# Kernel optimization log

Hardware: AMD Instinct MI355X
Metric: run time of the kernel (lower is better)

## Reference

```python
import jax, jax.numpy as jnp
import numpy as np

DELTA = 16
L_S = 32
HID = 8      # fast SSM hidden dim
GH = 64      # slow GRU hidden
OD = 2 * HID # slow branch output dim


def setup_inputs() -> dict:
    key = jax.random.key(0)
    ks = jax.random.split(key, 9)
    B, T = 128, 65536
    x = jax.random.normal(ks[0], (B, T), dtype=jnp.float32)
    # fast branch params: f_in: Linear(1, HID, bias=False); f_out: Linear(HID, 1, bias=False)
    w_in = jax.random.normal(ks[1], (HID,), dtype=jnp.float32) * 0.3
    w_out = jax.random.normal(ks[2], (HID,), dtype=jnp.float32) * 0.3
    # slow branch GRU (input_size=1) + output linear
    w_ih = jax.random.normal(ks[3], (3 * GH,), dtype=jnp.float32) * 0.1
    w_hh = jax.random.normal(ks[4], (3 * GH, GH), dtype=jnp.float32) * 0.1
    b_ih = jax.random.normal(ks[5], (3 * GH,), dtype=jnp.float32) * 0.1
    b_hh = jax.random.normal(ks[6], (3 * GH,), dtype=jnp.float32) * 0.1
    w_sl = jax.random.normal(ks[7], (OD, GH), dtype=jnp.float32) * 0.1
    b_sl = jax.random.normal(ks[8], (OD,), dtype=jnp.float32) * 0.1
    return {"x": x, "w_in": w_in, "w_out": w_out, "w_ih": w_ih, "w_hh": w_hh,
            "b_ih": b_ih, "b_hh": b_hh, "w_sl": w_sl, "b_sl": b_sl}


def _slow_branch(frames, w_ih, w_hh, b_ih, b_hh, w_sl, b_sl):
    # frames: (B, F, L_S). GRU over the L_S samples of each frame, last hidden -> Linear.
    B, F, L = frames.shape
    seq = frames.reshape(B * F, L).T  # (L, B*F), time-major

    def gru_step(h, xt):
        gi = xt[:, None] * w_ih[None, :] + b_ih          # (N, 3GH)
        gh = h @ w_hh.T + b_hh                            # (N, 3GH)
        ir, iz, inn = jnp.split(gi, 3, axis=-1)
        hr, hz, hn = jnp.split(gh, 3, axis=-1)
        r = jax.nn.sigmoid(ir + hr)
        z = jax.nn.sigmoid(iz + hz)
        n = jnp.tanh(inn + r * hn)
        h = (1.0 - z) * n + z * h
        return h, None

    h0 = jnp.zeros((B * F, GH), dtype=frames.dtype)
    hT, _ = jax.lax.scan(gru_step, h0, seq)
    eps = hT @ w_sl.T + b_sl                              # (B*F, OD)
    return eps.reshape(B, F, OD)


def reference(x, w_in, w_out, w_ih, w_hh, b_ih, b_hh, w_sl, b_sl):
    B, T = x.shape
    F = (T - L_S) // DELTA + 1
    # x.unfold(1, 32, delta) -> gather frames (B, F, L_S)
    idx = jnp.arange(F)[:, None] * DELTA + jnp.arange(L_S)[None, :]
    frames = x[:, idx]                                    # (B, F, L_S)
    eps = _slow_branch(frames, w_ih, w_hh, b_ih, b_hh, w_sl, b_sl)
    A_s = jax.nn.sigmoid(eps[..., :HID])                  # (B, F, H)
    g_s = eps[..., HID:]                                  # (B, F, H)
    # per-timestep frame index j = clamp(i // delta - 1, 0)
    j = jnp.clip(jnp.arange(T) // DELTA - 1, 0, F - 1)
    A_t = A_s[:, j]                                       # (B, T, H)
    g_t = g_s[:, j]                                       # (B, T, H)
    # x_emb = f_in(x) * g  (f_in has no bias)
    u_t = x[:, :, None] * w_in[None, None, :] * g_t       # (B, T, H)

    def step(h, inp):
        A, u = inp
        h = A * h + u
        return h, h

    h0 = jnp.zeros((B, HID), dtype=x.dtype)
    _, hs = jax.lax.scan(step, h0, (A_t.transpose(1, 0, 2), u_t.transpose(1, 0, 2)))  # hs: (T, B, H)
    y = jnp.einsum('tbh,h->bt', hs, w_out)                # f_out, no bias
    return y
```

## Files before the change

kernel.cpp:

```cpp
#include <hip/hip_runtime.h>
#include <hip/hip_bf16.h>
#include <math.h>

#define B_SZ 128
#define T_SZ 65536
#define F_FR 4095
#define GHID 64
#define HID 8
#define CHUNK 256
#define NCH (T_SZ / CHUNK)

typedef _Float16 half8 __attribute__((ext_vector_type(8)));
typedef float f32x4 __attribute__((ext_vector_type(4)));

#define L2E 1.4426950408889634f

static __device__ __forceinline__ float frcp(float v) {
#if __has_builtin(__builtin_amdgcn_rcpf)
    return __builtin_amdgcn_rcpf(v);
#else
    return 1.0f / v;
#endif
}
static __device__ __forceinline__ float fexp2(float v) {
#if __has_builtin(__builtin_amdgcn_exp2f)
    return __builtin_amdgcn_exp2f(v);
#else
    return exp2f(v);
#endif
}
__device__ __forceinline__ float sigm(float xv) { return frcp(1.0f + fexp2(-L2E * xv)); }

#define FSTR 68
#define XSTR 34

__global__ __launch_bounds__(256)
void gru_mfma(
    const float* __restrict__ x, const float* __restrict__ w_ih,
    const float* __restrict__ w_hh, const float* __restrict__ b_ih,
    const float* __restrict__ b_hh, const float* __restrict__ w_sl,
    const float* __restrict__ b_sl, float* __restrict__ ag)
{
    __shared__ _Float16 wlds[24 * 64 * 8];
    __shared__ float hx[4][32 * FSTR + 32 * XSTR];
    const int tid  = threadIdx.x;
    const int wv   = tid >> 6;
    const int lane = tid & 63;
    const int c16  = lane & 15;
    const int g    = lane >> 4;
    float* hb = &hx[wv][0];
    float* xs = hb + 32 * FSTR;
    const int tile = ((int)blockIdx.x * 4 + wv) * 32;

#pragma unroll
    for (int f = 0; f < 24; f += 4) {
        const int fi = f + wv;
        const int n = fi >> 1, c = fi & 1;
        const float sc = (n < 8) ? -L2E : (2.0f * L2E);
        const float* wp = w_hh + (16 * n + c16) * 64 + 32 * c + 8 * g;
        const float4 q0 = *(const float4*)wp;
        const float4 q1 = *(const float4*)(wp + 4);
        half8 w8;
        w8[0] = (_Float16)(sc * q0.x); w8[1] = (_Float16)(sc * q0.y);
        w8[2] = (_Float16)(sc * q0.z); w8[3] = (_Float16)(sc * q0.w);
        w8[4] = (_Float16)(sc * q1.x); w8[5] = (_Float16)(sc * q1.y);
        w8[6] = (_Float16)(sc * q1.z); w8[7] = (_Float16)(sc * q1.w);
        *(half8*)(wlds + (fi * 64 + lane) * 8) = w8;
    }

    float wiR[4], wiZ[4], wiN[4], bR[4], bZ[4], biN[4], bhN[4];
#pragma unroll
    for (int m = 0; m < 4; ++m) {
        const int j = c16 + 16 * m;
        wiR[m] = -L2E * w_ih[j];
        wiZ[m] = -L2E * w_ih[64 + j];
        wiN[m] = 2.0f * L2E * w_ih[128 + j];
        bR[m]  = -L2E * (b_ih[j] + b_hh[j]);
        bZ[m]  = -L2E * (b_ih[64 + j] + b_hh[64 + j]);
        biN[m] = 2.0f * L2E * b_ih[128 + j];
        bhN[m] = 2.0f * L2E * b_hh[128 + j];
    }

    {
        const int sl = lane & 31, half = lane >> 5;
        const int s = tile + sl;
        const int b = s / F_FR;
        const int f = s % F_FR;
        const float* xp = x + (long)b * T_SZ + f * 16 + 16 * half;
        const float4 p0 = *(const float4*)xp;
        const float4 p1 = *(const float4*)(xp + 4);
        const float4 p2 = *(const float4*)(xp + 8);
        const float4 p3 = *(const float4*)(xp + 12);
        float* xd = xs + sl * XSTR + 16 * half;
        *(float4*)(xd)      = p0;  *(float4*)(xd + 4)  = p1;
        *(float4*)(xd + 8)  = p2;  *(float4*)(xd + 12) = p3;
    }
    for (int idx = lane; idx < 32 * FSTR; idx += 64) hb[idx] = 0.0f;
    __syncthreads();

    float ho[2][4][4];
#pragma unroll
    for (int mt = 0; mt < 2; ++mt)
#pragma unroll
        for (int m = 0; m < 4; ++m)
#pragma unroll
            for (int r = 0; r < 4; ++r) ho[mt][m][r] = 0.0f;

#pragma unroll 1
    for (int t = 0; t < 32; ++t) {
        half8 ah[2][2], al[2][2];
#pragma unroll
        for (int mt = 0; mt < 2; ++mt)
#pragma unroll
        for (int c = 0; c < 2; ++c) {
            const float* rp = hb + (c16 + 16 * mt) * FSTR + 32 * c + 8 * g;
            const float4 u0 = *(const float4*)rp;
            const float4 u1 = *(const float4*)(rp + 4);
            const float fv[8] = {u0.x, u0.y, u0.z, u0.w, u1.x, u1.y, u1.z, u1.w};
#pragma unroll
            for (int e = 0; e < 8; ++e) {
                const _Float16 hi = (_Float16)fv[e];
                ah[mt][c][e] = hi;
                al[mt][c][e] = (_Float16)(fv[e] - (float)hi);
            }
        }
        float xt4[2][4];
#pragma unroll
        for (int mt = 0; mt < 2; ++mt)
#pragma unroll
        for (int r = 0; r < 4; ++r) xt4[mt][r] = xs[(4 * g + r + 16 * mt) * XSTR + t];

#pragma unroll
        for (int m = 0; m < 4; ++m) {
            f32x4 aR[2], aZ[2], aN[2];
#pragma unroll
            for (int mt = 0; mt < 2; ++mt) {
                aR[mt] = f32x4{bR[m], bR[m], bR[m], bR[m]};
                aZ[mt] = f32x4{bZ[m], bZ[m], bZ[m], bZ[m]};
                aN[mt] = f32x4{bhN[m], bhN[m], bhN[m], bhN[m]};
            }
#pragma unroll
            for (int c = 0; c < 2; ++c) {
                const half8 bfR = *(const half8*)(wlds + ((2 * m + c)       * 64 + lane) * 8);
                const half8 bfZ = *(const half8*)(wlds + ((2 * (4 + m) + c) * 64 + lane) * 8);
                const half8 bfN = *(const half8*)(wlds + ((2 * (8 + m) + c) * 64 + lane) * 8);
#pragma unroll
                for (int mt = 0; mt < 2; ++mt) {
                    aR[mt] = __builtin_amdgcn_mfma_f32_16x16x32_f16(ah[mt][c], bfR, aR[mt], 0, 0, 0);
                    aR[mt] = __builtin_amdgcn_mfma_f32_16x16x32_f16(al[mt][c], bfR, aR[mt], 0, 0, 0);
                    aZ[mt] = __builtin_amdgcn_mfma_f32_16x16x32_f16(ah[mt][c], bfZ, aZ[mt], 0, 0, 0);
                    aZ[mt] = __builtin_amdgcn_mfma_f32_16x16x32_f16(al[mt][c], bfZ, aZ[mt], 0, 0, 0);
                    aN[mt] = __builtin_amdgcn_mfma_f32_16x16x32_f16(ah[mt][c], bfN, aN[mt], 0, 0, 0);
                    aN[mt] = __builtin_amdgcn_mfma_f32_16x16x32_f16(al[mt][c], bfN, aN[mt], 0, 0, 0);
                }
            }
            const int jm = c16 + 16 * m;
#pragma unroll
            for (int mt = 0; mt < 2; ++mt) {
#pragma unroll
                for (int r = 0; r < 4; ++r) {
                    const float uR = fmaf(xt4[mt][r], wiR[m], aR[mt][r]);
                    const float rr = frcp(1.0f + fexp2(uR));
                    const float uZ = fmaf(xt4[mt][r], wiZ[m], aZ[mt][r]);
                    const float zf = frcp(1.0f + fexp2(uZ));
                    const float uN = fmaf(rr, aN[mt][r], fmaf(xt4[mt][r], wiN[m], biN[m]));
                    const float nn = fmaf(-2.0f, frcp(1.0f + fexp2(uN)), 1.0f);
                    const float hnew = fmaf(zf, ho[mt][m][r] - nn, nn);
                    ho[mt][m][r] = hnew;
                    hb[(4 * g + r + 16 * mt) * FSTR + jm] = hnew;
                }
            }
        }
    }

    const f32x4 zz = {0.0f, 0.0f, 0.0f, 0.0f};
    half8 wsl[2];
#pragma unroll
    for (int c = 0; c < 2; ++c) {
        const float4 q0 = *(const float4*)(w_sl + c16 * 64 + 32 * c + 8 * g);
        const float4 q1 = *(const float4*)(w_sl + c16 * 64 + 32 * c + 8 * g + 4);
        wsl[c][0] = (_Float16)q0.x; wsl[c][1] = (_Float16)q0.y;
        wsl[c][2] = (_Float16)q0.z; wsl[c][3] = (_Float16)q0.w;
        wsl[c][4] = (_Float16)q1.x; wsl[c][5] = (_Float16)q1.y;
        wsl[c][6] = (_Float16)q1.z; wsl[c][7] = (_Float16)q1.w;
    }
    const float bs = b_sl[c16];
#pragma unroll
    for (int mt = 0; mt < 2; ++mt) {
        half8 fh[2], fl[2];
#pragma unroll
        for (int c = 0; c < 2; ++c) {
            const float* rp = hb + (c16 + 16 * mt) * FSTR + 32 * c + 8 * g;
            const float4 u0 = *(const float4*)rp;
            const float4 u1 = *(const float4*)(rp + 4);
            const float fv[8] = {u0.x, u0.y, u0.z, u0.w, u1.x, u1.y, u1.z, u1.w};
#pragma unroll
            for (int e = 0; e < 8; ++e) {
                const _Float16 hi = (_Float16)fv[e];
                fh[c][e] = hi;
                fl[c][e] = (_Float16)(fv[e] - (float)hi);
            }
        }
        f32x4 ec = __builtin_amdgcn_mfma_f32_16x16x32_f16(fh[0], wsl[0], zz, 0, 0, 0);
        ec = __builtin_amdgcn_mfma_f32_16x16x32_f16(fl[0], wsl[0], ec, 0, 0, 0);
        ec = __builtin_amdgcn_mfma_f32_16x16x32_f16(fh[1], wsl[1], ec, 0, 0, 0);
        ec = __builtin_amdgcn_mfma_f32_16x16x32_f16(fl[1], wsl[1], ec, 0, 0, 0);
#pragma unroll
        for (int r = 0; r < 4; ++r) {
            float e = ec[r] + bs;
            if (c16 < 8) e = sigm(e);
            ag[(long)(tile + 16 * mt + 4 * g + r) * 16 + c16] = e;
        }
    }
}

__global__ __launch_bounds__(256) void fast_chunk(
    const float* __restrict__ x, const float* __restrict__ ag,
    const float* __restrict__ w_in,
    float* __restrict__ chP, float* __restrict__ chH)
{
    const int tid = blockIdx.x * 256 + threadIdx.x;
    const int b = tid / NCH, c = tid % NCH;
    float h[HID], P[HID];
#pragma unroll
    for (int i = 0; i < HID; ++i) { h[i] = 0.0f; P[i] = 1.0f; }
    const float* xp = x + (long)b * T_SZ + c * CHUNK;

#pragma unroll 1
    for (int g = 0; g < CHUNK / 16; ++g) {
        const int t0 = c * CHUNK + g * 16;
        int fr = t0 / 16 - 1; fr = max(0, min(F_FR - 1, fr));
        const float4* agp = (const float4*)(ag + ((long)b * F_FR + fr) * 16);
        const float4 a0 = agp[0], a1 = agp[1], g0 = agp[2], g1 = agp[3];
        const float A[HID]  = {a0.x, a0.y, a0.z, a0.w, a1.x, a1.y, a1.z, a1.w};
        const float Gv[HID] = {g0.x, g0.y, g0.z, g0.w, g1.x, g1.y, g1.z, g1.w};
        float wg[HID];
#pragma unroll
        for (int i = 0; i < HID; ++i) wg[i] = w_in[i] * Gv[i];
#pragma unroll
        for (int tt = 0; tt < 16; ++tt) {
            const float xt = xp[g * 16 + tt];
#pragma unroll
            for (int i = 0; i < HID; ++i) h[i] = fmaf(A[i], h[i], xt * wg[i]);
        }
#pragma unroll
        for (int i = 0; i < HID; ++i) {
            const float a2 = A[i] * A[i]; const float a4 = a2 * a2; const float a8 = a4 * a4;
            P[i] *= a8 * a8;
        }
    }
    float* pp = chP + (long)tid * HID;
    float* hp = chH + (long)tid * HID;
#pragma unroll
    for (int i = 0; i < HID; ++i) { pp[i] = P[i]; hp[i] = h[i]; }
}

__global__ __launch_bounds__(256) void chunk_scan(
    const float* __restrict__ chP, const float* __restrict__ chH,
    float* __restrict__ st)
{
    const int tid = blockIdx.x * 256 + threadIdx.x;
    if (tid >= B_SZ * HID) return;
    const int b = tid / HID, i = tid % HID;
    float h = 0.0f;
#pragma unroll 1
    for (int c = 0; c < NCH; ++c) {
        const long idx = ((long)b * NCH + c) * HID + i;
        st[idx] = h;
        h = fmaf(chP[idx], h, chH[idx]);
    }
}

__global__ __launch_bounds__(256) void fast_apply(
    const float* __restrict__ x, const float* __restrict__ ag,
    const float* __restrict__ w_in, const float* __restrict__ w_out,
    const float* __restrict__ st, float* __restrict__ y)
{
    const int tid = blockIdx.x * 256 + threadIdx.x;
    const int b = tid / NCH, c = tid % NCH;
    float h[HID];
    const float* sp = st + (long)tid * HID;
#pragma unroll
    for (int i = 0; i < HID; ++i) h[i] = sp[i];
    float wo[HID];
#pragma unroll
    for (int i = 0; i < HID; ++i) wo[i] = w_out[i];
    const float* xp = x + (long)b * T_SZ + c * CHUNK;
    float* yp = y + (long)b * T_SZ + c * CHUNK;

#pragma unroll 1
    for (int g = 0; g < CHUNK / 16; ++g) {
        const int t0 = c * CHUNK + g * 16;
        int fr = t0 / 16 - 1; fr = max(0, min(F_FR - 1, fr));
        const float4* agp = (const float4*)(ag + ((long)b * F_FR + fr) * 16);
        const float4 a0 = agp[0], a1 = agp[1], g0 = agp[2], g1 = agp[3];
        const float A[HID]  = {a0.x, a0.y, a0.z, a0.w, a1.x, a1.y, a1.z, a1.w};
        const float Gv[HID] = {g0.x, g0.y, g0.z, g0.w, g1.x, g1.y, g1.z, g1.w};
        float wg[HID];
#pragma unroll
        for (int i = 0; i < HID; ++i) wg[i] = w_in[i] * Gv[i];
#pragma unroll
        for (int tt = 0; tt < 16; ++tt) {
            const float xt = xp[g * 16 + tt];
            float acc = 0.0f;
#pragma unroll
            for (int i = 0; i < HID; ++i) {
                h[i] = fmaf(A[i], h[i], xt * wg[i]);
                acc = fmaf(h[i], wo[i], acc);
            }
            yp[g * 16 + tt] = acc;
        }
    }
}

extern "C" void kernel_launch(void* const* d_in, const int* in_sizes, int n_in,
                              void* d_out, int out_size, void* d_ws, size_t ws_size,
                              hipStream_t stream) {
    const float* x    = (const float*)d_in[0];
    const float* w_in = (const float*)d_in[1];
    const float* w_out= (const float*)d_in[2];
    const float* w_ih = (const float*)d_in[3];
    const float* w_hh = (const float*)d_in[4];
    const float* b_ih = (const float*)d_in[5];
    const float* b_hh = (const float*)d_in[6];
    const float* w_sl = (const float*)d_in[7];
    const float* b_sl = (const float*)d_in[8];
    float* y = (float*)d_out;

    float* ag  = (float*)d_ws;
    size_t off = (size_t)B_SZ * F_FR * 16;
    float* chP = ag + off;
    float* chH = chP + (size_t)B_SZ * NCH * HID;
    float* st  = chH + (size_t)B_SZ * NCH * HID;

    gru_mfma<<<4095, 256, 0, stream>>>(x, w_ih, w_hh, b_ih, b_hh, w_sl, b_sl, ag);
    fast_chunk<<<(B_SZ * NCH) / 256, 256, 0, stream>>>(x, ag, w_in, chP, chH);
    chunk_scan<<<(B_SZ * HID + 255) / 256, 256, 0, stream>>>(chP, chH, st);
    fast_apply<<<(B_SZ * NCH) / 256, 256, 0, stream>>>(x, ag, w_in, w_out, st, y);
}
```

Baseline: 1.410 ms.

## Drop split-fp16 GRU hidden state, keep h in fp16 LDS, 64 sequences per wave

The GRU kernel stops splitting the hidden state into hi/lo fp16 parts, which halves the MFMA count per step. The hidden state and input samples are now stored in LDS as fp16 with a permuted K-layout, so each step writes packed half4 values from registers. The input-projection term moves into the accumulator init. Each wave now processes 64 sequences instead of 32, with half as many blocks, launch bounds for 2 blocks per CU, and clamped and guarded tail handling. The cost is lower precision in the recurrent hidden state and input x, plus higher register pressure.

```diff
diff --git a/kernel.cpp b/kernel.cpp
--- a/kernel.cpp
+++ b/kernel.cpp
@@ -5,13 +5,15 @@
 #define B_SZ 128
 #define T_SZ 65536
 #define F_FR 4095
-#define GHID 64
+#define NSEQ (B_SZ * F_FR)
 #define HID 8
 #define CHUNK 256
 #define NCH (T_SZ / CHUNK)
 
-typedef _Float16 half8 __attribute__((ext_vector_type(8)));
-typedef float f32x4 __attribute__((ext_vector_type(4)));
+typedef _Float16 half8  __attribute__((ext_vector_type(8)));
+typedef _Float16 half4v __attribute__((ext_vector_type(4)));
+typedef __fp16   fp16x2 __attribute__((ext_vector_type(2)));
+typedef float    f32x4  __attribute__((ext_vector_type(4)));
 
 #define L2E 1.4426950408889634f
 
@@ -31,10 +33,10 @@
 }
 __device__ __forceinline__ float sigm(float xv) { return frcp(1.0f + fexp2(-L2E * xv)); }
 
-#define FSTR 68
-#define XSTR 34
-
-__global__ __launch_bounds__(256)
+#define HSTR 72
+#define XTSTR 68
+
+__global__ __launch_bounds__(256, 2)
 void gru_mfma(
     const float* __restrict__ x, const float* __restrict__ w_ih,
     const float* __restrict__ w_hh, const float* __restrict__ b_ih,
@@ -42,30 +44,28 @@
     const float* __restrict__ b_sl, float* __restrict__ ag)
 {
     __shared__ _Float16 wlds[24 * 64 * 8];
-    __shared__ float hx[4][32 * FSTR + 32 * XSTR];
+    __shared__ _Float16 hlds[4][64 * HSTR];
+    __shared__ _Float16 xlds[4][32 * XTSTR];
     const int tid  = threadIdx.x;
     const int wv   = tid >> 6;
     const int lane = tid & 63;
     const int c16  = lane & 15;
     const int g    = lane >> 4;
-    float* hb = &hx[wv][0];
-    float* xs = hb + 32 * FSTR;
-    const int tile = ((int)blockIdx.x * 4 + wv) * 32;
+    _Float16* hb = &hlds[wv][0];
+    _Float16* xw = &xlds[wv][0];
+    const int tile = ((int)blockIdx.x * 4 + wv) * 64;
 
 #pragma unroll
     for (int f = 0; f < 24; f += 4) {
         const int fi = f + wv;
         const int n = fi >> 1, c = fi & 1;
         const float sc = (n < 8) ? -L2E : (2.0f * L2E);
-        const float* wp = w_hh + (16 * n + c16) * 64 + 32 * c + 8 * g;
-        const float4 q0 = *(const float4*)wp;
-        const float4 q1 = *(const float4*)(wp + 4);
+        const float* wr = w_hh + (16 * n + c16) * 64 + 8 * c + 2 * g;
         half8 w8;
-        w8[0] = (_Float16)(sc * q0.x); w8[1] = (_Float16)(sc * q0.y);
-        w8[2] = (_Float16)(sc * q0.z); w8[3] = (_Float16)(sc * q0.w);
-        w8[4] = (_Float16)(sc * q1.x); w8[5] = (_Float16)(sc * q1.y);
-        w8[6] = (_Float16)(sc * q1.z); w8[7] = (_Float16)(sc * q1.w);
-        *(half8*)(wlds + (fi * 64 + lane) * 8) = w8;
+#pragma unroll
+        for (int e = 0; e < 8; ++e)
+            w8[e] = (_Float16)(sc * wr[(e & 3) * 16 + (e >> 2)]);
+        *(half8*)(wlds + fi * 512 + lane * 8) = w8;
     }
 
     float wiR[4], wiZ[4], wiN[4], bR[4], bZ[4], biN[4], bhN[4];
@@ -82,134 +82,120 @@
     }
 
     {
-        const int sl = lane & 31, half = lane >> 5;
-        const int s = tile + sl;
-        const int b = s / F_FR;
-        const int f = s % F_FR;
-        const float* xp = x + (long)b * T_SZ + f * 16 + 16 * half;
-        const float4 p0 = *(const float4*)xp;
-        const float4 p1 = *(const float4*)(xp + 4);
-        const float4 p2 = *(const float4*)(xp + 8);
-        const float4 p3 = *(const float4*)(xp + 12);
-        float* xd = xs + sl * XSTR + 16 * half;
-        *(float4*)(xd)      = p0;  *(float4*)(xd + 4)  = p1;
-        *(float4*)(xd + 8)  = p2;  *(float4*)(xd + 12) = p3;
-    }
-    for (int idx = lane; idx < 32 * FSTR; idx += 64) hb[idx] = 0.0f;
+        int sq = tile + lane; if (sq > NSEQ - 1) sq = NSEQ - 1;
+        const int b = sq / F_FR, fr = sq % F_FR;
+        const float* xp = x + (long)b * T_SZ + fr * 16;
+#pragma unroll
+        for (int t4 = 0; t4 < 32; t4 += 4) {
+            const float4 q = *(const float4*)(xp + t4);
+            xw[(t4 + 0) * XTSTR + lane] = (_Float16)q.x;
+            xw[(t4 + 1) * XTSTR + lane] = (_Float16)q.y;
+            xw[(t4 + 2) * XTSTR + lane] = (_Float16)q.z;
+            xw[(t4 + 3) * XTSTR + lane] = (_Float16)q.w;
+        }
+    }
+    {
+        uint32_t* hz = (uint32_t*)hb;
+#pragma unroll
+        for (int i = 0; i < 36; ++i) hz[lane + 64 * i] = 0;
+    }
     __syncthreads();
 
-    float ho[2][4][4];
-#pragma unroll
-    for (int mt = 0; mt < 2; ++mt)
-#pragma unroll
-        for (int m = 0; m < 4; ++m)
-#pragma unroll
-            for (int r = 0; r < 4; ++r) ho[mt][m][r] = 0.0f;
+    float ho[4][4][4];
+#pragma unroll
+    for (int m = 0; m < 4; ++m)
+#pragma unroll
+        for (int mt = 0; mt < 4; ++mt)
+#pragma unroll
+            for (int r = 0; r < 4; ++r) ho[m][mt][r] = 0.0f;
 
 #pragma unroll 1
     for (int t = 0; t < 32; ++t) {
-        half8 ah[2][2], al[2][2];
-#pragma unroll
-        for (int mt = 0; mt < 2; ++mt)
-#pragma unroll
-        for (int c = 0; c < 2; ++c) {
-            const float* rp = hb + (c16 + 16 * mt) * FSTR + 32 * c + 8 * g;
-            const float4 u0 = *(const float4*)rp;
-            const float4 u1 = *(const float4*)(rp + 4);
-            const float fv[8] = {u0.x, u0.y, u0.z, u0.w, u1.x, u1.y, u1.z, u1.w};
-#pragma unroll
-            for (int e = 0; e < 8; ++e) {
-                const _Float16 hi = (_Float16)fv[e];
-                ah[mt][c][e] = hi;
-                al[mt][c][e] = (_Float16)(fv[e] - (float)hi);
-            }
-        }
-        float xt4[2][4];
-#pragma unroll
-        for (int mt = 0; mt < 2; ++mt)
-#pragma unroll
-        for (int r = 0; r < 4; ++r) xt4[mt][r] = xs[(4 * g + r + 16 * mt) * XSTR + t];
+        half8 ah[4][2];
+#pragma unroll
+        for (int mt = 0; mt < 4; ++mt)
+#pragma unroll
+            for (int c = 0; c < 2; ++c)
+                ah[mt][c] = *(const half8*)(hb + (c16 + 16 * mt) * HSTR + 32 * c + 8 * g);
+        float xt[4][4];
+#pragma unroll
+        for (int mt = 0; mt < 4; ++mt) {
+            const half4v xv = *(const half4v*)(xw + t * XTSTR + 16 * mt + 4 * g);
+#pragma unroll
+            for (int r = 0; r < 4; ++r) xt[mt][r] = (float)xv[r];
+        }
 
 #pragma unroll
         for (int m = 0; m < 4; ++m) {
-            f32x4 aR[2], aZ[2], aN[2];
-#pragma unroll
-            for (int mt = 0; mt < 2; ++mt) {
-                aR[mt] = f32x4{bR[m], bR[m], bR[m], bR[m]};
-                aZ[mt] = f32x4{bZ[m], bZ[m], bZ[m], bZ[m]};
-                aN[mt] = f32x4{bhN[m], bhN[m], bhN[m], bhN[m]};
-            }
+            f32x4 aR[4], aZ[4], aN[4];
+#pragma unroll
+            for (int mt = 0; mt < 4; ++mt)
+#pragma unroll
+                for (int r = 0; r < 4; ++r) {
+                    aR[mt][r] = fmaf(xt[mt][r], wiR[m], bR[m]);
+                    aZ[mt][r] = fmaf(xt[mt][r], wiZ[m], bZ[m]);
+                    aN[mt][r] = bhN[m];
+                }
 #pragma unroll
             for (int c = 0; c < 2; ++c) {
-                const half8 bfR = *(const half8*)(wlds + ((2 * m + c)       * 64 + lane) * 8);
-                const half8 bfZ = *(const half8*)(wlds + ((2 * (4 + m) + c) * 64 + lane) * 8);
-                const half8 bfN = *(const half8*)(wlds + ((2 * (8 + m) + c) * 64 + lane) * 8);
-#pragma unroll
-                for (int mt = 0; mt < 2; ++mt) {
+                const half8 bfR = *(const half8*)(wlds + (2 * m + c)       * 512 + lane * 8);
+                const half8 bfZ = *(const half8*)(wlds + (2 * (4 + m) + c) * 512 + lane * 8);
+                const half8 bfN = *(const half8*)(wlds + (2 * (8 + m) + c) * 512 + lane * 8);
+#pragma unroll
+                for (int mt = 0; mt < 4; ++mt) {
                     aR[mt] = __builtin_amdgcn_mfma_f32_16x16x32_f16(ah[mt][c], bfR, aR[mt], 0, 0, 0);
-                    aR[mt] = __builtin_amdgcn_mfma_f32_16x16x32_f16(al[mt][c], bfR, aR[mt], 0, 0, 0);
                     aZ[mt] = __builtin_amdgcn_mfma_f32_16x16x32_f16(ah[mt][c], bfZ, aZ[mt], 0, 0, 0);
-                    aZ[mt] = __builtin_amdgcn_mfma_f32_16x16x32_f16(al[mt][c], bfZ, aZ[mt], 0, 0, 0);
                     aN[mt] = __builtin_amdgcn_mfma_f32_16x16x32_f16(ah[mt][c], bfN, aN[mt], 0, 0, 0);
-                    aN[mt] = __builtin_amdgcn_mfma_f32_16x16x32_f16(al[mt][c], bfN, aN[mt], 0, 0, 0);
                 }
             }
-            const int jm = c16 + 16 * m;
-#pragma unroll
-            for (int mt = 0; mt < 2; ++mt) {
+#pragma unroll
+            for (int mt = 0; mt < 4; ++mt)
 #pragma unroll
                 for (int r = 0; r < 4; ++r) {
-                    const float uR = fmaf(xt4[mt][r], wiR[m], aR[mt][r]);
-                    const float rr = frcp(1.0f + fexp2(uR));
-                    const float uZ = fmaf(xt4[mt][r], wiZ[m], aZ[mt][r]);
-                    const float zf = frcp(1.0f + fexp2(uZ));
-                    const float uN = fmaf(rr, aN[mt][r], fmaf(xt4[mt][r], wiN[m], biN[m]));
+                    const float rr = frcp(1.0f + fexp2(aR[mt][r]));
+                    const float zf = frcp(1.0f + fexp2(aZ[mt][r]));
+                    const float uN = fmaf(rr, aN[mt][r], fmaf(xt[mt][r], wiN[m], biN[m]));
                     const float nn = fmaf(-2.0f, frcp(1.0f + fexp2(uN)), 1.0f);
-                    const float hnew = fmaf(zf, ho[mt][m][r] - nn, nn);
-                    ho[mt][m][r] = hnew;
-                    hb[(4 * g + r + 16 * mt) * FSTR + jm] = hnew;
+                    ho[m][mt][r] = fmaf(zf, ho[m][mt][r] - nn, nn);
                 }
+        }
+
+#pragma unroll
+        for (int mt = 0; mt < 4; ++mt)
+#pragma unroll
+            for (int r = 0; r < 4; ++r) {
+                const fp16x2 p0 = __builtin_amdgcn_cvt_pkrtz(ho[0][mt][r], ho[1][mt][r]);
+                const fp16x2 p1 = __builtin_amdgcn_cvt_pkrtz(ho[2][mt][r], ho[3][mt][r]);
+                half4v hv;
+                hv.x = (_Float16)p0.x; hv.y = (_Float16)p0.y;
+                hv.z = (_Float16)p1.x; hv.w = (_Float16)p1.y;
+                *(half4v*)(hb + (4 * g + r + 16 * mt) * HSTR + 4 * c16) = hv;
             }
-        }
-    }
-
+    }
+
+    half8 wsl[2];
+#pragma unroll
+    for (int c = 0; c < 2; ++c) {
+        const float* wr = w_sl + c16 * 64 + 8 * c + 2 * g;
+#pragma unroll
+        for (int e = 0; e < 8; ++e) wsl[c][e] = (_Float16)wr[(e & 3) * 16 + (e >> 2)];
+    }
+    const float bs = b_sl[c16];
     const f32x4 zz = {0.0f, 0.0f, 0.0f, 0.0f};
-    half8 wsl[2];
-#pragma unroll
-    for (int c = 0; c < 2; ++c) {
-        const float4 q0 = *(const float4*)(w_sl + c16 * 64 + 32 * c + 8 * g);
-        const float4 q1 = *(const float4*)(w_sl + c16 * 64 + 32 * c + 8 * g + 4);
-        wsl[c][0] = (_Float16)q0.x; wsl[c][1] = (_Float16)q0.y;
-        wsl[c][2] = (_Float16)q0.z; wsl[c][3] = (_Float16)q0.w;
-        wsl[c][4] = (_Float16)q1.x; wsl[c][5] = (_Float16)q1.y;
-        wsl[c][6] = (_Float16)q1.z; wsl[c][7] = (_Float16)q1.w;
-    }
-    const float bs = b_sl[c16];
-#pragma unroll
-    for (int mt = 0; mt < 2; ++mt) {
-        half8 fh[2], fl[2];
-#pragma unroll
-        for (int c = 0; c < 2; ++c) {
-            const float* rp = hb + (c16 + 16 * mt) * FSTR + 32 * c + 8 * g;
-            const float4 u0 = *(const float4*)rp;
-            const float4 u1 = *(const float4*)(rp + 4);
-            const float fv[8] = {u0.x, u0.y, u0.z, u0.w, u1.x, u1.y, u1.z, u1.w};
-#pragma unroll
-            for (int e = 0; e < 8; ++e) {
-                const _Float16 hi = (_Float16)fv[e];
-                fh[c][e] = hi;
-                fl[c][e] = (_Float16)(fv[e] - (float)hi);
+#pragma unroll
+    for (int mt = 0; mt < 4; ++mt) {
+        const half8 fh0 = *(const half8*)(hb + (c16 + 16 * mt) * HSTR + 8 * g);
+        const half8 fh1 = *(const half8*)(hb + (c16 + 16 * mt) * HSTR + 32 + 8 * g);
+        f32x4 ec = __builtin_amdgcn_mfma_f32_16x16x32_f16(fh0, wsl[0], zz, 0, 0, 0);
+        ec = __builtin_amdgcn_mfma_f32_16x16x32_f16(fh1, wsl[1], ec, 0, 0, 0);
+#pragma unroll
+        for (int r = 0; r < 4; ++r) {
+            const int s = tile + 16 * mt + 4 * g + r;
+            if (s < NSEQ) {
+                float e = ec[r] + bs;
+                if (c16 < 8) e = sigm(e);
+                ag[(long)s * 16 + c16] = e;
             }
-        }
-        f32x4 ec = __builtin_amdgcn_mfma_f32_16x16x32_f16(fh[0], wsl[0], zz, 0, 0, 0);
-        ec = __builtin_amdgcn_mfma_f32_16x16x32_f16(fl[0], wsl[0], ec, 0, 0, 0);
-        ec = __builtin_amdgcn_mfma_f32_16x16x32_f16(fh[1], wsl[1], ec, 0, 0, 0);
-        ec = __builtin_amdgcn_mfma_f32_16x16x32_f16(fl[1], wsl[1], ec, 0, 0, 0);
-#pragma unroll
-        for (int r = 0; r < 4; ++r) {
-            float e = ec[r] + bs;
-            if (c16 < 8) e = sigm(e);
-            ag[(long)(tile + 16 * mt + 4 * g + r) * 16 + c16] = e;
         }
     }
 }
@@ -333,7 +319,7 @@
     float* chH = chP + (size_t)B_SZ * NCH * HID;
     float* st  = chH + (size_t)B_SZ * NCH * HID;
 
-    gru_mfma<<<4095, 256, 0, stream>>>(x, w_ih, w_hh, b_ih, b_hh, w_sl, b_sl, ag);
+    gru_mfma<<<2048, 256, 0, stream>>>(x, w_ih, w_hh, b_ih, b_hh, w_sl, b_sl, ag);
     fast_chunk<<<(B_SZ * NCH) / 256, 256, 0, stream>>>(x, ag, w_in, chP, chH);
     chunk_scan<<<(B_SZ * HID + 255) / 256, 256, 0, stream>>>(chP, chH, st);
     fast_apply<<<(B_SZ * NCH) / 256, 256, 0, stream>>>(x, ag, w_in, w_out, st, y);
```

Result: slower. 2.182 ms (+54.7%).
